# Optimization experiments

Measured on AMD Instinct MI355X. Metric: run time of the kernel, lower is better.

The kernel has to match this reference:

```python
import jax, jax.numpy as jnp
import numpy as np

N_NODES = 50000
D = 128
N_EDGES = 800000


def _gcn_layer(h, W, b, row, col, mask, n_nodes):
    # Linear: h @ W.T + b  (nn.Linear convention)
    h = h @ W.T + b
    # degree of source nodes, counting only non-self-loop edges (remove_self_loops)
    deg = jax.ops.segment_sum(mask.astype(h.dtype), row, num_segments=n_nodes)
    deg_inv_sqrt = jnp.where(deg > 0, jax.lax.rsqrt(jnp.maximum(deg, 1.0)), 0.0)
    norm = deg_inv_sqrt[row] * deg_inv_sqrt[col] * mask.astype(h.dtype)
    # gather-scale messages [E, D], scatter-add into target nodes (col)
    msg = norm[:, None] * h[row]
    return jax.ops.segment_sum(msg, col, num_segments=n_nodes)


def setup_inputs() -> dict:
    key = jax.random.key(0)
    ks = jax.random.split(key, 9)
    x = jax.random.normal(ks[0], (N_NODES, D), dtype=jnp.float32)
    edge_index = jax.random.randint(ks[1], (2, N_EDGES), 0, N_NODES, dtype=jnp.int64)
    lim = 1.0 / np.sqrt(D)
    params = {}
    for i in range(3):
        params[f"W{i}"] = jax.random.uniform(ks[2 + 2 * i], (D, D), jnp.float32, -lim, lim)
        params[f"b{i}"] = jax.random.uniform(ks[3 + 2 * i], (D,), jnp.float32, -lim, lim)
    return {"x": x, "edge_index": edge_index, **params}


def reference(x, edge_index, W0, b0, W1, b1, W2, b2):
    row, col = edge_index[0], edge_index[1]
    mask = row != col  # remove_self_loops
    h = x
    for W, b in ((W0, b0), (W1, b1), (W2, b2)):
        h_new = jax.nn.relu(_gcn_layer(h, W, b, row, col, mask, x.shape[0]))
        h = h + h_new
    return h
```

## Files before the change

kernel.cpp:

```cpp
#include <hip/hip_runtime.h>
#include <hip/hip_bf16.h>


#define D_DIM 128
#define SCAN_CHUNK 1024
#define CHUNKS 256
#define GROUPS 8
#define GS (CHUNKS / GROUPS)
#define LDSW 12512

typedef __attribute__((ext_vector_type(8))) short bf16x8;
typedef __attribute__((ext_vector_type(4))) float f32x4;

static __device__ __forceinline__ short f2bf(float f) {
    union { __hip_bfloat16 b; short s; } u;
    u.b = __float2bfloat16(f);
    return u.s;
}
static __device__ __forceinline__ float bf_lo(unsigned p) { return __uint_as_float(p << 16); }
static __device__ __forceinline__ float bf_hi(unsigned p) { return __uint_as_float(p & 0xffff0000u); }


__global__ __launch_bounds__(256) void hist_kernel(const int* __restrict__ ei,
                                                   unsigned* __restrict__ partial_col,
                                                   unsigned* __restrict__ partial_row,
                                                   int E, int CHSZ) {
    __shared__ unsigned hh[LDSW];
    int tid = threadIdx.x;
    int ch = blockIdx.x;
    int docol = (blockIdx.y == 0);
    for (int i = tid; i < LDSW; i += 256) hh[i] = 0u;
    __syncthreads();
    int e0 = ch * CHSZ, e1 = min(e0 + CHSZ, E);
    for (int e = e0 + tid; e < e1; e += 256) {
        int row = ei[e];
        int col = ei[E + e];
        if (row == col) continue;
        int bin = docol ? col : row;
        atomicAdd(&hh[bin >> 2], 1u << ((bin & 3) * 8));
    }
    __syncthreads();
    unsigned* dst = (docol ? partial_col : partial_row) + (size_t)ch * LDSW;
    for (int i = tid; i < LDSW; i += 256) dst[i] = hh[i];
}

__global__ __launch_bounds__(256) void group_prefix_kernel(
    unsigned* __restrict__ partial_col, const unsigned* __restrict__ partial_row,
    unsigned* __restrict__ gsum_col, unsigned* __restrict__ gsum_row, int NW) {
    int w = blockIdx.x * 256 + threadIdx.x;
    if (w >= NW) return;
    int g = blockIdx.y;
    size_t base = (size_t)(g * GS) * LDSW + w;
    if (blockIdx.z == 0) {
        unsigned run = 0;
#pragma unroll 4
        for (int c = 0; c < GS; c++) {
            unsigned v = partial_col[base + (size_t)c * LDSW];
            partial_col[base + (size_t)c * LDSW] = run;
            run += v;
        }
        gsum_col[g * NW + w] = run;
    } else {
        unsigned run = 0;
#pragma unroll 4
        for (int c = 0; c < GS; c++) run += partial_row[base + (size_t)c * LDSW];
        gsum_row[g * NW + w] = run;
    }
}

__global__ __launch_bounds__(256) void cnt_dis_kernel(
    const unsigned* __restrict__ gsum_col, const unsigned* __restrict__ gsum_row,
    int* __restrict__ col_cnt, float* __restrict__ dis, int* __restrict__ bsum, int NW) {
    __shared__ int wsum[4];
    int w = blockIdx.x * 256 + threadIdx.x;
    int s = 0;
    if (w < NW) {
        unsigned clo = 0, chi = 0, rlo = 0, rhi = 0;
#pragma unroll
        for (int g = 0; g < GROUPS; g++) {
            unsigned wc = gsum_col[g * NW + w];
            unsigned wr = gsum_row[g * NW + w];
            clo += wc & 0x00FF00FFu; chi += (wc >> 8) & 0x00FF00FFu;
            rlo += wr & 0x00FF00FFu; rhi += (wr >> 8) & 0x00FF00FFu;
        }
        int c0 = clo & 0xFFFF, c1 = chi & 0xFFFF, c2 = clo >> 16, c3 = chi >> 16;
        int r0 = rlo & 0xFFFF, r1 = rhi & 0xFFFF, r2 = rlo >> 16, r3 = rhi >> 16;
        ((int4*)col_cnt)[w] = make_int4(c0, c1, c2, c3);
        float4 dv;
        dv.x = (r0 > 0) ? rsqrtf((float)r0) : 0.0f;
        dv.y = (r1 > 0) ? rsqrtf((float)r1) : 0.0f;
        dv.z = (r2 > 0) ? rsqrtf((float)r2) : 0.0f;
        dv.w = (r3 > 0) ? rsqrtf((float)r3) : 0.0f;
        ((float4*)dis)[w] = dv;
        s = c0 + c1 + c2 + c3;
    }
#pragma unroll
    for (int d = 32; d > 0; d >>= 1) s += __shfl_down(s, d, 64);
    int lane = threadIdx.x & 63, wv = threadIdx.x >> 6;
    if (lane == 0) wsum[wv] = s;
    __syncthreads();
    if (threadIdx.x == 0) bsum[blockIdx.x] = wsum[0] + wsum[1] + wsum[2] + wsum[3];
}

__global__ __launch_bounds__(64) void scan_bbase_kernel(const int* __restrict__ bsum,
                                                        int* __restrict__ bbase,
                                                        int* __restrict__ offs,
                                                        int G, int n) {
    int lane = threadIdx.x;
    int v = (lane < G) ? bsum[lane] : 0;
    int s = v;
#pragma unroll
    for (int d = 1; d < 64; d <<= 1) {
        int t = __shfl_up(s, d, 64);
        if (lane >= d) s += t;
    }
    if (lane < G) bbase[lane] = s - v;
    if (lane == 63) offs[n] = s;
}

__global__ __launch_bounds__(256) void scan_final_kernel(const int* __restrict__ cnt,
                                                         const int* __restrict__ bbase,
                                                         int* __restrict__ offs, int n) {
    __shared__ int wsum[4];
    int base = blockIdx.x * SCAN_CHUNK;
    int tid = threadIdx.x;
    const int PT = SCAN_CHUNK / 256;
    int v[PT];
    int s = 0;
#pragma unroll
    for (int i = 0; i < PT; i++) {
        int g = base + tid * PT + i;
        v[i] = (g < n) ? cnt[g] : 0;
        s += v[i];
    }
    int local_sum = s;
    int lane = tid & 63, w = tid >> 6;
#pragma unroll
    for (int d = 1; d < 64; d <<= 1) {
        int t = __shfl_up(s, d, 64);
        if (lane >= d) s += t;
    }
    if (lane == 63) wsum[w] = s;
    __syncthreads();
    int wbase = 0;
    for (int i = 0; i < w; i++) wbase += wsum[i];
    int run = bbase[blockIdx.x] + wbase + (s - local_sum);
#pragma unroll
    for (int i = 0; i < PT; i++) {
        int g = base + tid * PT + i;
        if (g < n) offs[g] = run;
        run += v[i];
    }
}

__global__ __launch_bounds__(256) void group_base_kernel(
    unsigned* __restrict__ partial_col, const unsigned* __restrict__ gsum_col, int NW) {
    int w = blockIdx.x * 256 + threadIdx.x;
    if (w >= NW) return;
    int g = blockIdx.y + 1;
    unsigned gb = 0;
    for (int gp = 0; gp < g; gp++) gb += gsum_col[gp * NW + w];
    size_t base = (size_t)(g * GS) * LDSW + w;
#pragma unroll 4
    for (int c = 0; c < GS; c++) partial_col[base + (size_t)c * LDSW] += gb;
}

__global__ __launch_bounds__(256) void scatter_kernel(const int* __restrict__ ei,
                                                      const float* __restrict__ dis,
                                                      const int* __restrict__ offs,
                                                      const unsigned* __restrict__ chpref,
                                                      int2* __restrict__ epack,
                                                      int E, int CHSZ) {
    __shared__ unsigned cur[LDSW];
    int tid = threadIdx.x;
    int ch = blockIdx.x;
    for (int i = tid; i < LDSW; i += 256) cur[i] = 0u;
    __syncthreads();
    int e0 = ch * CHSZ, e1 = min(e0 + CHSZ, E);
    const unsigned* pf = chpref + (size_t)ch * LDSW;
    for (int e = e0 + tid; e < e1; e += 256) {
        int row = ei[e];
        int col = ei[E + e];
        if (row == col) continue;
        float wgt = dis[row] * dis[col];
        int wd = col >> 2, sh = (col & 3) * 8;
        unsigned old = atomicAdd(&cur[wd], 1u << sh);
        int slot = offs[col] + (int)((pf[wd] >> sh) & 0xFFu) + (int)((old >> sh) & 0xFFu);
        epack[slot] = make_int2(row * (D_DIM / 2), __float_as_int(wgt));
    }
}

__global__ void wcvt_all_kernel(const float* __restrict__ W0, const float* __restrict__ W1,
                                const float* __restrict__ W2, unsigned short* __restrict__ B0,
                                unsigned short* __restrict__ B1, unsigned short* __restrict__ B2) {
    int i = blockIdx.x * blockDim.x + threadIdx.x;
    const float* W = (blockIdx.y == 0) ? W0 : (blockIdx.y == 1) ? W1 : W2;
    unsigned short* B = (blockIdx.y == 0) ? B0 : (blockIdx.y == 1) ? B1 : B2;
    if (i < D_DIM * D_DIM) B[i] = (unsigned short)f2bf(W[i]);
}


__global__ __launch_bounds__(256) void linear_mfma_kernel(
    const float* __restrict__ A, const unsigned short* __restrict__ Wb,
    const float* __restrict__ bias, unsigned short* __restrict__ hWb, int nrows) {
    int wave = threadIdx.x >> 6;
    int lane = threadIdx.x & 63;
    int r0 = blockIdx.x * 64 + wave * 16;
    int m = lane & 15, q = lane >> 4;
    int rload = min(r0 + m, nrows - 1);
    const float4* h4 = (const float4*)A;

    f32x4 acc[8];
#pragma unroll
    for (int jt = 0; jt < 8; jt++) acc[jt] = (f32x4){0.f, 0.f, 0.f, 0.f};

#pragma unroll
    for (int k0 = 0; k0 < 128; k0 += 32) {
        int c0 = k0 + q * 8;
        float4 x0 = h4[rload * 32 + (c0 >> 2)];
        float4 x1 = h4[rload * 32 + (c0 >> 2) + 1];
        bf16x8 a;
        a[0] = f2bf(x0.x); a[1] = f2bf(x0.y); a[2] = f2bf(x0.z); a[3] = f2bf(x0.w);
        a[4] = f2bf(x1.x); a[5] = f2bf(x1.y); a[6] = f2bf(x1.z); a[7] = f2bf(x1.w);
#pragma unroll
        for (int jt = 0; jt < 8; jt++) {
            bf16x8 b = *(const bf16x8*)(Wb + (jt * 16 + m) * D_DIM + c0);
            acc[jt] = __builtin_amdgcn_mfma_f32_16x16x32_bf16(a, b, acc[jt], 0, 0, 0);
        }
    }

#pragma unroll
    for (int jt = 0; jt < 8; jt++) {
        int col = jt * 16 + m;
        float bv = bias[col];
#pragma unroll
        for (int reg = 0; reg < 4; reg++) {
            int rr = r0 + q * 4 + reg;
            if (rr < nrows) hWb[(size_t)rr * D_DIM + col] = (unsigned short)f2bf(acc[jt][reg] + bv);
        }
    }
}

__global__ __launch_bounds__(256) void agg_kernel(const int* __restrict__ offs,
                                                  const int2* __restrict__ epack,
                                                  const unsigned int* __restrict__ hW2,
                                                  const float* __restrict__ hprev,
                                                  float* __restrict__ hout, int n_nodes) {
    int node = (int)((blockIdx.x * blockDim.x + threadIdx.x) >> 6);
    int lane = threadIdx.x & 63;
    if (node >= n_nodes) return;

    int beg = offs[node];
    int end = offs[node + 1];

    float ax8[8], ay8[8];
#pragma unroll
    for (int u = 0; u < 8; u++) { ax8[u] = 0.f; ay8[u] = 0.f; }

    int i = beg;
    for (; i + 8 <= end; i += 8) {
        int2 e[8];
        unsigned p[8];
#pragma unroll
        for (int u = 0; u < 8; u++) e[u] = epack[i + u];
#pragma unroll
        for (int u = 0; u < 8; u++) p[u] = hW2[e[u].x + lane];
#pragma unroll
        for (int u = 0; u < 8; u++) {
            float w = __int_as_float(e[u].y);
            ax8[u] = fmaf(w, bf_lo(p[u]), ax8[u]);
            ay8[u] = fmaf(w, bf_hi(p[u]), ay8[u]);
        }
    }
    int rem = end - i;
    if (rem & 4) {
        int2 e[4];
        unsigned p[4];
#pragma unroll
        for (int u = 0; u < 4; u++) e[u] = epack[i + u];
#pragma unroll
        for (int u = 0; u < 4; u++) p[u] = hW2[e[u].x + lane];
#pragma unroll
        for (int u = 0; u < 4; u++) {
            float w = __int_as_float(e[u].y);
            ax8[u] = fmaf(w, bf_lo(p[u]), ax8[u]);
            ay8[u] = fmaf(w, bf_hi(p[u]), ay8[u]);
        }
        i += 4;
    }
    if (rem & 2) {
        int2 e0 = epack[i], e1 = epack[i + 1];
        unsigned p0 = hW2[e0.x + lane], p1 = hW2[e1.x + lane];
        float w0 = __int_as_float(e0.y), w1 = __int_as_float(e1.y);
        ax8[4] = fmaf(w0, bf_lo(p0), ax8[4]); ay8[4] = fmaf(w0, bf_hi(p0), ay8[4]);
        ax8[5] = fmaf(w1, bf_lo(p1), ax8[5]); ay8[5] = fmaf(w1, bf_hi(p1), ay8[5]);
        i += 2;
    }
    if (rem & 1) {
        int2 e0 = epack[i];
        unsigned p0 = hW2[e0.x + lane];
        float w0 = __int_as_float(e0.y);
        ax8[6] = fmaf(w0, bf_lo(p0), ax8[6]); ay8[6] = fmaf(w0, bf_hi(p0), ay8[6]);
    }
    float ax = ((ax8[0] + ax8[1]) + (ax8[2] + ax8[3])) + ((ax8[4] + ax8[5]) + (ax8[6] + ax8[7]));
    float ay = ((ay8[0] + ay8[1]) + (ay8[2] + ay8[3])) + ((ay8[4] + ay8[5]) + (ay8[6] + ay8[7]));

    int idx = node * (D_DIM / 2) + lane;
    float2 hv = ((const float2*)hprev)[idx];
    float2 o;
    o.x = hv.x + fmaxf(ax, 0.0f);
    o.y = hv.y + fmaxf(ay, 0.0f);
    ((float2*)hout)[idx] = o;
}


static inline size_t align_up(size_t x, size_t a) { return (x + a - 1) & ~(a - 1); }

extern "C" void kernel_launch(void* const* d_in, const int* in_sizes, int n_in,
                              void* d_out, int out_size, void* d_ws, size_t ws_size,
                              hipStream_t stream) {
    const float* x = (const float*)d_in[0];
    const int* ei = (const int*)d_in[1];
    const float* Wl[3] = {(const float*)d_in[2], (const float*)d_in[4], (const float*)d_in[6]};
    const float* bl[3] = {(const float*)d_in[3], (const float*)d_in[5], (const float*)d_in[7]};

    const int N = in_sizes[0] / D_DIM;
    const int E = in_sizes[1] / 2;
    const int NW = N / 4;
    const int G = (N + SCAN_CHUNK - 1) / SCAN_CHUNK;
    const int NWB = (NW + 255) / 256;
    const int CHSZ = (E + CHUNKS - 1) / CHUNKS;

    char* p = (char*)d_ws;
    int* col_cnt = (int*)p;            p += align_up((size_t)N * 4, 256);
    int* offs    = (int*)p;            p += align_up((size_t)(N + 1) * 4, 256);
    float* dis   = (float*)p;          p += align_up((size_t)N * 4, 256);
    int* bsum    = (int*)p;            p += align_up((size_t)64 * 4, 256);
    int* bbase   = (int*)p;            p += align_up((size_t)64 * 4, 256);
    unsigned* partial_col = (unsigned*)p;  p += align_up((size_t)CHUNKS * LDSW * 4, 256);
    unsigned* partial_row = (unsigned*)p;  p += align_up((size_t)CHUNKS * LDSW * 4, 256);
    unsigned* gsum_col = (unsigned*)p; p += align_up((size_t)GROUPS * NW * 4, 256);
    unsigned* gsum_row = (unsigned*)p; p += align_up((size_t)GROUPS * NW * 4, 256);
    unsigned short* Wb[3];
    for (int l = 0; l < 3; l++) { Wb[l] = (unsigned short*)p; p += align_up((size_t)D_DIM * D_DIM * 2, 256); }
    int2* epack  = (int2*)p;           p += align_up((size_t)E * 8, 256);
    unsigned short* hWb = (unsigned short*)p;  p += align_up((size_t)N * D_DIM * 2, 256);
    (void)ws_size;

    hist_kernel<<<dim3(CHUNKS, 2), 256, 0, stream>>>(ei, partial_col, partial_row, E, CHSZ);
    group_prefix_kernel<<<dim3(NWB, GROUPS, 2), 256, 0, stream>>>(partial_col, partial_row,
                                                                  gsum_col, gsum_row, NW);
    cnt_dis_kernel<<<NWB, 256, 0, stream>>>(gsum_col, gsum_row, col_cnt, dis, bsum, NW);
    scan_bbase_kernel<<<1, 64, 0, stream>>>(bsum, bbase, offs, G, N);
    scan_final_kernel<<<G, 256, 0, stream>>>(col_cnt, bbase, offs, N);
    group_base_kernel<<<dim3(NWB, GROUPS - 1), 256, 0, stream>>>(partial_col, gsum_col, NW);
    scatter_kernel<<<CHUNKS, 256, 0, stream>>>(ei, dis, offs, partial_col, epack, E, CHSZ);
    wcvt_all_kernel<<<dim3((D_DIM * D_DIM + 255) / 256, 3), 256, 0, stream>>>(
        Wl[0], Wl[1], Wl[2], Wb[0], Wb[1], Wb[2]);

    const float* hprev = x;
    float* h = (float*)d_out;
    int gemm_blocks = (N + 63) / 64;
    int agg_blocks = (N + 3) / 4;
    for (int l = 0; l < 3; l++) {
        linear_mfma_kernel<<<gemm_blocks, 256, 0, stream>>>(hprev, Wb[l], bl[l], hWb, N);
        agg_kernel<<<agg_blocks, 256, 0, stream>>>(offs, epack, (const unsigned int*)hWb, hprev, h, N);
        hprev = h;
    }
}
```

Measured before the change: 326.4 us.

## Fuse weight conversion and all GCN layers into one persistent cooperative kernel

Replaces the per-layer GEMM and aggregation launches, plus the weight conversion kernel, with a single cooperative persistent kernel that separates phases with grid-wide syncs. The GEMM epilogue now stages bf16 outputs in LDS so each row is written with 16-byte stores instead of scattered 2-byte stores. Edge and feature streams use nontemporal loads and stores. This removes six launch gaps, but adds grid.sync costs and fixes occupancy to a persistent grid with grid-stride loops, which can give worse load balance than one wave per node.

```diff
diff --git a/kernel.cpp b/kernel.cpp
--- a/kernel.cpp
+++ b/kernel.cpp
@@ -1,5 +1,8 @@
 #include <hip/hip_runtime.h>
 #include <hip/hip_bf16.h>
+#include <hip/hip_cooperative_groups.h>
+
+namespace cg = cooperative_groups;
 
 
 #define D_DIM 128
@@ -19,6 +22,8 @@
 }
 static __device__ __forceinline__ float bf_lo(unsigned p) { return __uint_as_float(p << 16); }
 static __device__ __forceinline__ float bf_hi(unsigned p) { return __uint_as_float(p & 0xffff0000u); }
+
+union f2ll { float2 f; long long ll; };
 
 
 __global__ __launch_bounds__(256) void hist_kernel(const int* __restrict__ ei,
@@ -190,127 +195,153 @@
     }
 }
 
-__global__ void wcvt_all_kernel(const float* __restrict__ W0, const float* __restrict__ W1,
-                                const float* __restrict__ W2, unsigned short* __restrict__ B0,
-                                unsigned short* __restrict__ B1, unsigned short* __restrict__ B2) {
-    int i = blockIdx.x * blockDim.x + threadIdx.x;
-    const float* W = (blockIdx.y == 0) ? W0 : (blockIdx.y == 1) ? W1 : W2;
-    unsigned short* B = (blockIdx.y == 0) ? B0 : (blockIdx.y == 1) ? B1 : B2;
-    if (i < D_DIM * D_DIM) B[i] = (unsigned short)f2bf(W[i]);
-}
-
-
-__global__ __launch_bounds__(256) void linear_mfma_kernel(
-    const float* __restrict__ A, const unsigned short* __restrict__ Wb,
-    const float* __restrict__ bias, unsigned short* __restrict__ hWb, int nrows) {
-    int wave = threadIdx.x >> 6;
-    int lane = threadIdx.x & 63;
-    int r0 = blockIdx.x * 64 + wave * 16;
+
+struct LayerParams {
+    const float* x;
+    const float* W0; const float* W1; const float* W2;
+    const float* b0; const float* b1; const float* b2;
+    const int* offs;
+    const long long* epack;
+    unsigned short* Wb;
+    unsigned short* hWb;
+    float* h;
+    int N;
+};
+
+__global__ __launch_bounds__(256, 4) void layers_kernel(LayerParams P) {
+    cg::grid_group grid = cg::this_grid();
+    __shared__ unsigned short stage[4][16 * 136];
+
+    int tid = threadIdx.x;
+    int lane = tid & 63, wv = tid >> 6;
     int m = lane & 15, q = lane >> 4;
-    int rload = min(r0 + m, nrows - 1);
-    const float4* h4 = (const float4*)A;
-
-    f32x4 acc[8];
-#pragma unroll
-    for (int jt = 0; jt < 8; jt++) acc[jt] = (f32x4){0.f, 0.f, 0.f, 0.f};
-
-#pragma unroll
-    for (int k0 = 0; k0 < 128; k0 += 32) {
-        int c0 = k0 + q * 8;
-        float4 x0 = h4[rload * 32 + (c0 >> 2)];
-        float4 x1 = h4[rload * 32 + (c0 >> 2) + 1];
-        bf16x8 a;
-        a[0] = f2bf(x0.x); a[1] = f2bf(x0.y); a[2] = f2bf(x0.z); a[3] = f2bf(x0.w);
-        a[4] = f2bf(x1.x); a[5] = f2bf(x1.y); a[6] = f2bf(x1.z); a[7] = f2bf(x1.w);
-#pragma unroll
-        for (int jt = 0; jt < 8; jt++) {
-            bf16x8 b = *(const bf16x8*)(Wb + (jt * 16 + m) * D_DIM + c0);
-            acc[jt] = __builtin_amdgcn_mfma_f32_16x16x32_bf16(a, b, acc[jt], 0, 0, 0);
+    int gthreads = (int)gridDim.x * 256;
+    int gtid = (int)blockIdx.x * 256 + tid;
+    int nwaves = (int)gridDim.x * 4;
+    int gwave = (int)blockIdx.x * 4 + wv;
+    int T = (P.N + 15) / 16;
+
+    for (int i = gtid; i < 3 * D_DIM * D_DIM; i += gthreads) {
+        const float* W = (i < 16384) ? P.W0 : (i < 32768) ? P.W1 : P.W2;
+        P.Wb[i] = (unsigned short)f2bf(W[i & 16383]);
+    }
+    grid.sync();
+
+    const float* hp = P.x;
+    for (int l = 0; l < 3; l++) {
+        const unsigned short* Wb = P.Wb + l * 16384;
+        const float* bias = (l == 0) ? P.b0 : (l == 1) ? P.b1 : P.b2;
+
+        for (int tile = gwave; tile < T; tile += nwaves) {
+            int r0 = tile * 16;
+            int rload = min(r0 + m, P.N - 1);
+            const float4* h4 = (const float4*)hp;
+            f32x4 acc[8];
+#pragma unroll
+            for (int jt = 0; jt < 8; jt++) acc[jt] = (f32x4){0.f, 0.f, 0.f, 0.f};
+#pragma unroll
+            for (int k0 = 0; k0 < 128; k0 += 32) {
+                int c0 = k0 + q * 8;
+                float4 x0 = h4[rload * 32 + (c0 >> 2)];
+                float4 x1 = h4[rload * 32 + (c0 >> 2) + 1];
+                bf16x8 a;
+                a[0] = f2bf(x0.x); a[1] = f2bf(x0.y); a[2] = f2bf(x0.z); a[3] = f2bf(x0.w);
+                a[4] = f2bf(x1.x); a[5] = f2bf(x1.y); a[6] = f2bf(x1.z); a[7] = f2bf(x1.w);
+#pragma unroll
+                for (int jt = 0; jt < 8; jt++) {
+                    bf16x8 b = *(const bf16x8*)(Wb + (jt * 16 + m) * D_DIM + c0);
+                    acc[jt] = __builtin_amdgcn_mfma_f32_16x16x32_bf16(a, b, acc[jt], 0, 0, 0);
+                }
+            }
+#pragma unroll
+            for (int jt = 0; jt < 8; jt++) {
+                float bv = bias[jt * 16 + m];
+#pragma unroll
+                for (int reg = 0; reg < 4; reg++)
+                    stage[wv][(q * 4 + reg) * 136 + jt * 16 + m] =
+                        (unsigned short)f2bf(acc[jt][reg] + bv);
+            }
+#pragma unroll
+            for (int t = 0; t < 4; t++) {
+                int rl = t * 4 + (lane >> 4);
+                int gr = r0 + rl;
+                if (gr < P.N) {
+                    uint4 v = *(const uint4*)&stage[wv][rl * 136 + (lane & 15) * 8];
+                    *(uint4*)&P.hWb[(size_t)gr * D_DIM + (lane & 15) * 8] = v;
+                }
+            }
         }
-    }
-
-#pragma unroll
-    for (int jt = 0; jt < 8; jt++) {
-        int col = jt * 16 + m;
-        float bv = bias[col];
-#pragma unroll
-        for (int reg = 0; reg < 4; reg++) {
-            int rr = r0 + q * 4 + reg;
-            if (rr < nrows) hWb[(size_t)rr * D_DIM + col] = (unsigned short)f2bf(acc[jt][reg] + bv);
+        grid.sync();
+
+        const unsigned* hW2 = (const unsigned*)P.hWb;
+        for (int node = gwave; node < P.N; node += nwaves) {
+            int beg = P.offs[node];
+            int end = P.offs[node + 1];
+            float ax8[8], ay8[8];
+#pragma unroll
+            for (int u = 0; u < 8; u++) { ax8[u] = 0.f; ay8[u] = 0.f; }
+            int i = beg;
+            for (; i + 8 <= end; i += 8) {
+                long long e[8];
+                unsigned p[8];
+#pragma unroll
+                for (int u = 0; u < 8; u++) e[u] = __builtin_nontemporal_load(P.epack + i + u);
+#pragma unroll
+                for (int u = 0; u < 8; u++) p[u] = hW2[(int)(e[u] & 0xffffffffLL) + lane];
+#pragma unroll
+                for (int u = 0; u < 8; u++) {
+                    float w = __int_as_float((int)(e[u] >> 32));
+                    ax8[u] = fmaf(w, bf_lo(p[u]), ax8[u]);
+                    ay8[u] = fmaf(w, bf_hi(p[u]), ay8[u]);
+                }
+            }
+            int rem = end - i;
+            if (rem & 4) {
+                long long e[4];
+                unsigned p[4];
+#pragma unroll
+                for (int u = 0; u < 4; u++) e[u] = __builtin_nontemporal_load(P.epack + i + u);
+#pragma unroll
+                for (int u = 0; u < 4; u++) p[u] = hW2[(int)(e[u] & 0xffffffffLL) + lane];
+#pragma unroll
+                for (int u = 0; u < 4; u++) {
+                    float w = __int_as_float((int)(e[u] >> 32));
+                    ax8[u] = fmaf(w, bf_lo(p[u]), ax8[u]);
+                    ay8[u] = fmaf(w, bf_hi(p[u]), ay8[u]);
+                }
+                i += 4;
+            }
+            if (rem & 2) {
+                long long e0 = __builtin_nontemporal_load(P.epack + i);
+                long long e1 = __builtin_nontemporal_load(P.epack + i + 1);
+                unsigned p0 = hW2[(int)(e0 & 0xffffffffLL) + lane];
+                unsigned p1 = hW2[(int)(e1 & 0xffffffffLL) + lane];
+                float w0 = __int_as_float((int)(e0 >> 32));
+                float w1 = __int_as_float((int)(e1 >> 32));
+                ax8[4] = fmaf(w0, bf_lo(p0), ax8[4]); ay8[4] = fmaf(w0, bf_hi(p0), ay8[4]);
+                ax8[5] = fmaf(w1, bf_lo(p1), ax8[5]); ay8[5] = fmaf(w1, bf_hi(p1), ay8[5]);
+                i += 2;
+            }
+            if (rem & 1) {
+                long long e0 = __builtin_nontemporal_load(P.epack + i);
+                unsigned p0 = hW2[(int)(e0 & 0xffffffffLL) + lane];
+                float w0 = __int_as_float((int)(e0 >> 32));
+                ax8[6] = fmaf(w0, bf_lo(p0), ax8[6]); ay8[6] = fmaf(w0, bf_hi(p0), ay8[6]);
+            }
+            float ax = ((ax8[0] + ax8[1]) + (ax8[2] + ax8[3])) + ((ax8[4] + ax8[5]) + (ax8[6] + ax8[7]));
+            float ay = ((ay8[0] + ay8[1]) + (ay8[2] + ay8[3])) + ((ay8[4] + ay8[5]) + (ay8[6] + ay8[7]));
+
+            int idx = node * (D_DIM / 2) + lane;
+            f2ll hin;
+            hin.ll = __builtin_nontemporal_load((const long long*)hp + idx);
+            f2ll o;
+            o.f.x = hin.f.x + fmaxf(ax, 0.0f);
+            o.f.y = hin.f.y + fmaxf(ay, 0.0f);
+            __builtin_nontemporal_store(o.ll, (long long*)P.h + idx);
         }
-    }
-}
-
-__global__ __launch_bounds__(256) void agg_kernel(const int* __restrict__ offs,
-                                                  const int2* __restrict__ epack,
-                                                  const unsigned int* __restrict__ hW2,
-                                                  const float* __restrict__ hprev,
-                                                  float* __restrict__ hout, int n_nodes) {
-    int node = (int)((blockIdx.x * blockDim.x + threadIdx.x) >> 6);
-    int lane = threadIdx.x & 63;
-    if (node >= n_nodes) return;
-
-    int beg = offs[node];
-    int end = offs[node + 1];
-
-    float ax8[8], ay8[8];
-#pragma unroll
-    for (int u = 0; u < 8; u++) { ax8[u] = 0.f; ay8[u] = 0.f; }
-
-    int i = beg;
-    for (; i + 8 <= end; i += 8) {
-        int2 e[8];
-        unsigned p[8];
-#pragma unroll
-        for (int u = 0; u < 8; u++) e[u] = epack[i + u];
-#pragma unroll
-        for (int u = 0; u < 8; u++) p[u] = hW2[e[u].x + lane];
-#pragma unroll
-        for (int u = 0; u < 8; u++) {
-            float w = __int_as_float(e[u].y);
-            ax8[u] = fmaf(w, bf_lo(p[u]), ax8[u]);
-            ay8[u] = fmaf(w, bf_hi(p[u]), ay8[u]);
-        }
-    }
-    int rem = end - i;
-    if (rem & 4) {
-        int2 e[4];
-        unsigned p[4];
-#pragma unroll
-        for (int u = 0; u < 4; u++) e[u] = epack[i + u];
-#pragma unroll
-        for (int u = 0; u < 4; u++) p[u] = hW2[e[u].x + lane];
-#pragma unroll
-        for (int u = 0; u < 4; u++) {
-            float w = __int_as_float(e[u].y);
-            ax8[u] = fmaf(w, bf_lo(p[u]), ax8[u]);
-            ay8[u] = fmaf(w, bf_hi(p[u]), ay8[u]);
-        }
-        i += 4;
-    }
-    if (rem & 2) {
-        int2 e0 = epack[i], e1 = epack[i + 1];
-        unsigned p0 = hW2[e0.x + lane], p1 = hW2[e1.x + lane];
-        float w0 = __int_as_float(e0.y), w1 = __int_as_float(e1.y);
-        ax8[4] = fmaf(w0, bf_lo(p0), ax8[4]); ay8[4] = fmaf(w0, bf_hi(p0), ay8[4]);
-        ax8[5] = fmaf(w1, bf_lo(p1), ax8[5]); ay8[5] = fmaf(w1, bf_hi(p1), ay8[5]);
-        i += 2;
-    }
-    if (rem & 1) {
-        int2 e0 = epack[i];
-        unsigned p0 = hW2[e0.x + lane];
-        float w0 = __int_as_float(e0.y);
-        ax8[6] = fmaf(w0, bf_lo(p0), ax8[6]); ay8[6] = fmaf(w0, bf_hi(p0), ay8[6]);
-    }
-    float ax = ((ax8[0] + ax8[1]) + (ax8[2] + ax8[3])) + ((ax8[4] + ax8[5]) + (ax8[6] + ax8[7]));
-    float ay = ((ay8[0] + ay8[1]) + (ay8[2] + ay8[3])) + ((ay8[4] + ay8[5]) + (ay8[6] + ay8[7]));
-
-    int idx = node * (D_DIM / 2) + lane;
-    float2 hv = ((const float2*)hprev)[idx];
-    float2 o;
-    o.x = hv.x + fmaxf(ax, 0.0f);
-    o.y = hv.y + fmaxf(ay, 0.0f);
-    ((float2*)hout)[idx] = o;
+        grid.sync();
+        hp = P.h;
+    }
 }
 
 
@@ -341,8 +372,7 @@
     unsigned* partial_row = (unsigned*)p;  p += align_up((size_t)CHUNKS * LDSW * 4, 256);
     unsigned* gsum_col = (unsigned*)p; p += align_up((size_t)GROUPS * NW * 4, 256);
     unsigned* gsum_row = (unsigned*)p; p += align_up((size_t)GROUPS * NW * 4, 256);
-    unsigned short* Wb[3];
-    for (int l = 0; l < 3; l++) { Wb[l] = (unsigned short*)p; p += align_up((size_t)D_DIM * D_DIM * 2, 256); }
+    unsigned short* Wb = (unsigned short*)p;  p += align_up((size_t)3 * D_DIM * D_DIM * 2, 256);
     int2* epack  = (int2*)p;           p += align_up((size_t)E * 8, 256);
     unsigned short* hWb = (unsigned short*)p;  p += align_up((size_t)N * D_DIM * 2, 256);
     (void)ws_size;
@@ -355,16 +385,23 @@
     scan_final_kernel<<<G, 256, 0, stream>>>(col_cnt, bbase, offs, N);
     group_base_kernel<<<dim3(NWB, GROUPS - 1), 256, 0, stream>>>(partial_col, gsum_col, NW);
     scatter_kernel<<<CHUNKS, 256, 0, stream>>>(ei, dis, offs, partial_col, epack, E, CHSZ);
-    wcvt_all_kernel<<<dim3((D_DIM * D_DIM + 255) / 256, 3), 256, 0, stream>>>(
-        Wl[0], Wl[1], Wl[2], Wb[0], Wb[1], Wb[2]);
-
-    const float* hprev = x;
-    float* h = (float*)d_out;
-    int gemm_blocks = (N + 63) / 64;
-    int agg_blocks = (N + 3) / 4;
-    for (int l = 0; l < 3; l++) {
-        linear_mfma_kernel<<<gemm_blocks, 256, 0, stream>>>(hprev, Wb[l], bl[l], hWb, N);
-        agg_kernel<<<agg_blocks, 256, 0, stream>>>(offs, epack, (const unsigned int*)hWb, hprev, h, N);
-        hprev = h;
-    }
-}
+
+    int occ = 0;
+    hipOccupancyMaxActiveBlocksPerMultiprocessor(&occ, layers_kernel, 256, 0);
+    if (occ < 1) occ = 1;
+    int lgrid = occ * 256;
+    if (lgrid > 2048) lgrid = 2048;
+
+    LayerParams prm;
+    prm.x = x;
+    prm.W0 = Wl[0]; prm.W1 = Wl[1]; prm.W2 = Wl[2];
+    prm.b0 = bl[0]; prm.b1 = bl[1]; prm.b2 = bl[2];
+    prm.offs = offs;
+    prm.epack = (const long long*)epack;
+    prm.Wb = Wb;
+    prm.hWb = hWb;
+    prm.h = (float*)d_out;
+    prm.N = N;
+    void* kp[] = { &prm };
+    hipLaunchCooperativeKernel(layers_kernel, dim3(lgrid), dim3(256), kp, 0, stream);
+}
```

Result: slower. 903.0 us (+176.7%).
